# Kernel tuning notes

Measured on AMD Instinct MI355X. Metric: run time of the kernel, lower is better.

The kernel has to match this reference:

```python
import jax, jax.numpy as jnp
import numpy as np

B, T, F, H = 4, 2048, 512, 8
DK = F // H


def setup_inputs() -> dict:
    key = jax.random.key(0)
    ks = jax.random.split(key, 12)
    s = 1.0 / np.sqrt(F)
    return {
        "query": jax.random.normal(ks[0], (B, T, F), jnp.float32),
        "key": jax.random.normal(ks[1], (B, T, F), jnp.float32),
        "value": jax.random.normal(ks[2], (B, T, F), jnp.float32),
        "attn_mask": jax.random.randint(ks[3], (B, 1, T), 0, 2, jnp.int32),
        "Wq": jax.random.uniform(ks[4], (F, F), jnp.float32, -s, s),
        "bq": jax.random.uniform(ks[5], (F,), jnp.float32, -s, s),
        "Wk": jax.random.uniform(ks[6], (F, F), jnp.float32, -s, s),
        "bk": jax.random.uniform(ks[7], (F,), jnp.float32, -s, s),
        "Wv": jax.random.uniform(ks[8], (F, F), jnp.float32, -s, s),
        "bv": jax.random.uniform(ks[9], (F,), jnp.float32, -s, s),
        "Wo": jax.random.uniform(ks[10], (F, F), jnp.float32, -s, s),
        "bo": jax.random.uniform(ks[11], (F,), jnp.float32, -s, s),
    }


def reference(query, key, value, attn_mask, Wq, bq, Wk, bk, Wv, bv, Wo, bo):
    b = query.shape[0]
    # QKV projections -> (b, h, t, d_k)
    q = (query @ Wq.T + bq).reshape(b, -1, H, DK).transpose(0, 2, 1, 3)
    k = (key @ Wk.T + bk).reshape(b, -1, H, DK).transpose(0, 2, 1, 3)
    v = (value @ Wv.T + bv).reshape(b, -1, H, DK).transpose(0, 2, 1, 3)
    scores = jnp.einsum("bhqd,bhkd->bhqk", q, k) / np.sqrt(DK)
    # mask (b,1,t2) -> (b,1,1,t2); masked where mask == 0
    m = (attn_mask[:, None, :, :] == 0)
    min_val = jnp.finfo(scores.dtype).min
    scores = jnp.where(m, min_val, scores)
    attn = jnp.where(m, 0.0, jax.nn.softmax(scores, axis=-1))
    # dropout is identity in eval mode
    x = jnp.einsum("bhqk,bhkd->bhqd", attn, v)
    x = x.transpose(0, 2, 1, 3).reshape(b, -1, H * DK)
    return x @ Wo.T + bo
```

## Files before the change

kernel.cpp:

```cpp
#include <hip/hip_runtime.h>
#include <hip/hip_bf16.h>
#include <stdint.h>

#define B_ 4
#define T_ 2048
#define F_ 512
#define H_ 8
#define DK_ 64
#define BT_ (B_*T_)

typedef short bf16x8 __attribute__((ext_vector_type(8)));
typedef short s16x4 __attribute__((ext_vector_type(4)));
typedef float f32x4 __attribute__((ext_vector_type(4)));
typedef float f32x16 __attribute__((ext_vector_type(16)));

__device__ __forceinline__ unsigned short f2bf(float f) {
  union { float f; unsigned u; } v; v.f = f;
  return (unsigned short)((v.u + 0x7fffu + ((v.u >> 16) & 1u)) >> 16);
}

__device__ __forceinline__ unsigned cvtpk(float lo, float hi) {
  unsigned w;
  asm("v_cvt_pk_bf16_f32 %0, %1, %2" : "=v"(w) : "v"(lo), "v"(hi));
  return w;
}

__device__ __forceinline__ void gload_lds16(const void* g, void* l) {
  __builtin_amdgcn_global_load_lds((const __attribute__((address_space(1))) void*)g,
                                   (__attribute__((address_space(3))) void*)l, 16, 0, 0);
}

__global__ void convert_scan(const float* __restrict__ wq, const float* __restrict__ wk,
                             const float* __restrict__ wv, const float* __restrict__ wo,
                             const int* __restrict__ mask,
                             unsigned short* __restrict__ dst, int* __restrict__ invidx,
                             int* __restrict__ nbuf, float* __restrict__ maskf) {
  const int seg = blockIdx.y;
  const int tid = threadIdx.x;
  if (seg == 4) {
    if (blockIdx.x >= 4) return;
    const int b = blockIdx.x;
    __shared__ int cnt[256];
    const int base = b * T_ + tid * 8;
    int4 a = *(const int4*)(mask + base);
    int4 d = *(const int4*)(mask + base + 4);
    int m[8] = {a.x, a.y, a.z, a.w, d.x, d.y, d.z, d.w};
    int c = 0;
#pragma unroll
    for (int i = 0; i < 8; ++i) c += (m[i] != 0);
    cnt[tid] = c;
    __syncthreads();
    for (int off = 1; off < 256; off <<= 1) {
      int v = (tid >= off) ? cnt[tid - off] : 0;
      __syncthreads();
      cnt[tid] += v;
      __syncthreads();
    }
    int excl = cnt[tid] - c;
#pragma unroll
    for (int i = 0; i < 8; ++i)
      if (m[i]) { invidx[b * T_ + excl] = tid * 8 + i; ++excl; }
    const int nb = cnt[255];
    if (tid == 255) nbuf[b] = nb;
#pragma unroll
    for (int i = 0; i < 8; ++i) {
      const int j = tid * 8 + i;
      maskf[b * T_ + j] = (j < nb) ? 0.0f : -__builtin_inff();
    }
    return;
  }
  const float* src = seg == 0 ? wq : (seg == 1 ? wk : (seg == 2 ? wv : wo));
  unsigned short* out = dst + (size_t)seg * F_ * F_;
  const int idx = (blockIdx.x * 256 + tid) * 8;
  float4 a = *(const float4*)(src + idx);
  float4 b = *(const float4*)(src + idx + 4);
  union { unsigned w[4]; bf16x8 v; } t;
  t.w[0] = cvtpk(a.x, a.y); t.w[1] = cvtpk(a.z, a.w);
  t.w[2] = cvtpk(b.x, b.y); t.w[3] = cvtpk(b.z, b.w);
  *(bf16x8*)(out + idx) = t.v;
}

__global__ __launch_bounds__(256, 3) void gemm_qkv(
    const float* __restrict__ qin, const float* __restrict__ kin, const float* __restrict__ vin,
    const unsigned short* __restrict__ Wbase,
    const float* __restrict__ bq, const float* __restrict__ bk, const float* __restrict__ bv,
    const int* __restrict__ invidx, const int* __restrict__ nbuf,
    unsigned short* __restrict__ projq, unsigned short* __restrict__ kc,
    unsigned short* __restrict__ vt, float qscale) {
  const int id = blockIdx.x;
  const int p = id >> 8, l = id & 255;
  const int tid = threadIdx.x;
  const int wid = tid >> 6, lane = tid & 63;
  const int lr = lane & 15, lg = lane >> 4;
  const int wr = wid >> 1, wc = wid & 1;
  const int n0 = (l & 3) * 128;

  const float* Af;
  const float* bias;
  float sc = 1.0f;
  int obase, j0 = 0, b = 0, nb = T_;
  if (p == 0) {
    obase = (l >> 2) * 128;
    Af = qin; bias = bq; sc = qscale;
  } else {
    b = l >> 6;
    j0 = ((l >> 2) & 15) * 128;
    nb = nbuf[b];
    if (j0 >= ((nb + 63) & ~63)) return;
    obase = b * T_ + j0;
    Af = (p == 1) ? kin : vin;
    bias = (p == 1) ? bk : bv;
  }
  const unsigned short* W = Wbase + (size_t)p * F_ * F_;

  __shared__ __align__(16) unsigned short As[128 * 64];
  __shared__ __align__(16) unsigned short Bs[128 * 64];

  int srcrow[4];
#pragma unroll
  for (int i = 0; i < 4; ++i) {
    const int r = (i * 256 + tid) >> 3;
    if (p == 0) srcrow[i] = obase + r;
    else {
      int j = j0 + r;
      if (j >= nb) j = nb - 1;
      srcrow[i] = b * T_ + invidx[b * T_ + j];
    }
  }

  float4 aR[4][2];
  auto loadA = [&](int k0) {
#pragma unroll
    for (int i = 0; i < 4; ++i) {
      const int s = (i * 256 + tid) & 7;
      const float* sp = Af + (size_t)srcrow[i] * F_ + k0 + s * 8;
      aR[i][0] = *(const float4*)sp;
      aR[i][1] = *(const float4*)(sp + 4);
    }
  };
  auto writeA = [&]() {
#pragma unroll
    for (int i = 0; i < 4; ++i) {
      const int ch = i * 256 + tid;
      const int r = ch >> 3, s = ch & 7;
      union { unsigned w[4]; bf16x8 v; } t;
      t.w[0] = cvtpk(aR[i][0].x, aR[i][0].y); t.w[1] = cvtpk(aR[i][0].z, aR[i][0].w);
      t.w[2] = cvtpk(aR[i][1].x, aR[i][1].y); t.w[3] = cvtpk(aR[i][1].z, aR[i][1].w);
      *(bf16x8*)&As[r * 64 + ((s ^ (r & 7)) * 8)] = t.v;
    }
  };
  auto stageB = [&](int k0) {
#pragma unroll
    for (int i = 0; i < 4; ++i) {
      const int ch = i * 256 + tid;
      const int r = ch >> 3, s = ch & 7;
      gload_lds16(W + (size_t)(n0 + r) * F_ + k0 + ((s ^ (r & 7)) * 8),
                  &Bs[(i * 256 + wid * 64) * 8]);
    }
  };

  f32x4 acc[4][4] = {};
  loadA(0);
  for (int k0 = 0; k0 < F_; k0 += 64) {
    stageB(k0);
    writeA();
    __syncthreads();
    if (k0 + 64 < F_) loadA(k0 + 64);

#pragma unroll
    for (int kk = 0; kk < 2; ++kk) {
      bf16x8 af[4], bf[4];
      const int slotA = (kk * 4 + lg) ^ (lr & 7);
#pragma unroll
      for (int m = 0; m < 4; ++m)
        af[m] = *(const bf16x8*)&As[(wr * 64 + m * 16 + lr) * 64 + slotA * 8];
#pragma unroll
      for (int n = 0; n < 4; ++n)
        bf[n] = *(const bf16x8*)&Bs[(wc * 64 + n * 16 + lr) * 64 + slotA * 8];
#pragma unroll
      for (int m = 0; m < 4; ++m)
#pragma unroll
        for (int n = 0; n < 4; ++n)
          acc[m][n] = __builtin_amdgcn_mfma_f32_16x16x32_bf16(af[m], bf[n], acc[m][n], 0, 0, 0);
    }
    __syncthreads();
  }

  if (p == 2) {
#pragma unroll
    for (int n = 0; n < 4; ++n) {
      const int col = n0 + wc * 64 + n * 16 + lr;
      const float bvv = bias[col];
      unsigned short* vrow = vt + ((size_t)(b * 8 + (col >> 6)) * 64 + (col & 63)) * T_;
#pragma unroll
      for (int m = 0; m < 4; ++m) {
        const int kv = j0 + wr * 64 + m * 16 + lg * 4;
        union { unsigned short u[4]; s16x4 v; } ov;
#pragma unroll
        for (int j = 0; j < 4; ++j) ov.u[j] = f2bf(acc[m][n][j] + bvv);
        *(s16x4*)(vrow + kv) = ov.v;
      }
    }
  } else {
    unsigned short* outp = (p == 0) ? projq : kc;
#pragma unroll
    for (int n = 0; n < 4; ++n) {
      const int col = n0 + wc * 64 + n * 16 + lr;
      const float bvv = bias[col];
#pragma unroll
      for (int m = 0; m < 4; ++m) {
        const int rbase = obase + wr * 64 + m * 16 + lg * 4;
#pragma unroll
        for (int j = 0; j < 4; ++j)
          outp[(size_t)(rbase + j) * F_ + col] = f2bf((acc[m][n][j] + bvv) * sc);
      }
    }
  }
}

__global__ __launch_bounds__(256, 3) void gemm_out(
    const unsigned short* __restrict__ Abf, const unsigned short* __restrict__ W,
    const float* __restrict__ bias, float* __restrict__ outf) {
  const int l = blockIdx.x;
  const int m0 = (l >> 2) * 128, n0 = (l & 3) * 128;
  const int tid = threadIdx.x;
  const int wid = tid >> 6, lane = tid & 63;
  const int lr = lane & 15, lg = lane >> 4;
  const int wr = wid >> 1, wc = wid & 1;

  __shared__ __align__(16) unsigned short As[128 * 64];
  __shared__ __align__(16) unsigned short Bs[128 * 64];

  auto stage = [&](int k0) {
#pragma unroll
    for (int i = 0; i < 4; ++i) {
      const int ch = i * 256 + tid;
      const int r = ch >> 3, s = ch & 7;
      const int ks = ((s ^ (r & 7)) * 8);
      gload_lds16(Abf + (size_t)(m0 + r) * F_ + k0 + ks, &As[(i * 256 + wid * 64) * 8]);
      gload_lds16(W + (size_t)(n0 + r) * F_ + k0 + ks, &Bs[(i * 256 + wid * 64) * 8]);
    }
  };

  f32x4 acc[4][4] = {};
  for (int k0 = 0; k0 < F_; k0 += 64) {
    stage(k0);
    __syncthreads();
#pragma unroll
    for (int kk = 0; kk < 2; ++kk) {
      bf16x8 af[4], bf[4];
      const int slotA = (kk * 4 + lg) ^ (lr & 7);
#pragma unroll
      for (int m = 0; m < 4; ++m)
        af[m] = *(const bf16x8*)&As[(wr * 64 + m * 16 + lr) * 64 + slotA * 8];
#pragma unroll
      for (int n = 0; n < 4; ++n)
        bf[n] = *(const bf16x8*)&Bs[(wc * 64 + n * 16 + lr) * 64 + slotA * 8];
#pragma unroll
      for (int m = 0; m < 4; ++m)
#pragma unroll
        for (int n = 0; n < 4; ++n)
          acc[m][n] = __builtin_amdgcn_mfma_f32_16x16x32_bf16(af[m], bf[n], acc[m][n], 0, 0, 0);
    }
    __syncthreads();
  }

#pragma unroll
  for (int n = 0; n < 4; ++n) {
    const int col = n0 + wc * 64 + n * 16 + lr;
    const float bvv = bias[col];
#pragma unroll
    for (int m = 0; m < 4; ++m) {
      const int rbase = m0 + wr * 64 + m * 16 + lg * 4;
#pragma unroll
      for (int j = 0; j < 4; ++j)
        outf[(size_t)(rbase + j) * F_ + col] = acc[m][n][j] + bvv;
    }
  }
}

__global__ __launch_bounds__(256, 2) void attn_kernel(
    const unsigned short* __restrict__ Qp,
    const unsigned short* __restrict__ Kp,
    const unsigned short* __restrict__ Vt,
    const float* __restrict__ maskf,
    const int* __restrict__ nbuf,
    unsigned short* __restrict__ X) {
  const int tid = threadIdx.x, wid = tid >> 6, lane = tid & 63;
  const int la = lane & 31, hi = lane >> 5;
  const int id = blockIdx.x;
  const int swz = (id & 7) * 64 + (id >> 3);
  const int bh = swz >> 4, qb = swz & 15;
  const int b = bh >> 3, h = bh & 7;
  const int qrow = qb * 128 + wid * 32 + la;
  const int nt = (nbuf[b] + 127) >> 7;

  __shared__ __align__(16) unsigned short Ks[2][128 * 64];
  __shared__ __align__(16) unsigned short Vs[2][64 * 128];
  __shared__ __align__(16) float Ms[2][128];

  bf16x8 qf[4];
#pragma unroll
  for (int kk = 0; kk < 4; ++kk)
    qf[kk] = *(const bf16x8*)(Qp + (size_t)(b * T_ + qrow) * F_ + h * DK_ + kk * 16 + hi * 8);

  f32x16 oacc[2] = {};
  float mrun = -1e30f, lrun = 0.0f;

  auto stage = [&](int buf, int kv0) {
#pragma unroll
    for (int i = 0; i < 4; ++i) {
      const int ch = i * 256 + tid;
      const int r = ch >> 3, s = ch & 7;
      gload_lds16(Kp + (size_t)(b * T_ + kv0 + r) * F_ + h * DK_ + ((s ^ (r & 7)) * 8),
                  &Ks[buf][(i * 256 + wid * 64) * 8]);
      const int d = ch >> 4, s2 = ch & 15;
      gload_lds16(Vt + ((size_t)bh * DK_ + d) * T_ + kv0 + ((s2 ^ (d & 15)) * 8),
                  &Vs[buf][(i * 256 + wid * 64) * 8]);
    }
    if (wid == 0 && lane < 32)
      gload_lds16(maskf + b * T_ + kv0 + lane * 4, &Ms[buf][0]);
  };

  if (nt > 0) {
    stage(0, 0);
    __syncthreads();

    for (int t = 0; t < nt; ++t) {
      const int cur = t & 1;
      if (t < nt - 1) stage(cur ^ 1, (t + 1) * 128);

      f32x16 sb[4];
      __builtin_amdgcn_s_setprio(1);
#pragma unroll
      for (int n = 0; n < 4; ++n) {
        bf16x8 kf[4];
#pragma unroll
        for (int kk = 0; kk < 4; ++kk)
          kf[kk] = *(const bf16x8*)&Ks[cur][(n * 32 + la) * 64 + ((((kk << 1) | hi) ^ (la & 7)) * 8)];
        f32x16 s = {};
#pragma unroll
        for (int kk = 0; kk < 4; ++kk)
          s = __builtin_amdgcn_mfma_f32_32x32x16_bf16(kf[kk], qf[kk], s, 0, 0, 0);
        sb[n] = s;
      }
      __builtin_amdgcn_s_setprio(0);

      f32x4 mfv[4][4];
#pragma unroll
      for (int n = 0; n < 4; ++n)
#pragma unroll
        for (int g = 0; g < 4; ++g)
          mfv[n][g] = *(const f32x4*)&Ms[cur][n * 32 + 8 * g + 4 * hi];

      float mx[16];
#pragma unroll
      for (int r = 0; r < 16; ++r)
        mx[r] = fmaxf(fmaxf(sb[0][r], sb[1][r]), fmaxf(sb[2][r], sb[3][r]));
#pragma unroll
      for (int st = 8; st > 0; st >>= 1)
#pragma unroll
        for (int r = 0; r < st; ++r) mx[r] = fmaxf(mx[r], mx[r + st]);
      const float rmx = fmaxf(mx[0], __shfl_xor(mx[0], 32, 64));

      if (!__all(rmx <= mrun + 8.0f)) {
        const float mnew = fmaxf(mrun, rmx);
        const float alpha = __builtin_amdgcn_exp2f(mrun - mnew);
        lrun *= alpha;
#pragma unroll
        for (int m = 0; m < 2; ++m)
#pragma unroll
          for (int r = 0; r < 16; ++r) oacc[m][r] *= alpha;
        mrun = mnew;
      }

#pragma unroll
      for (int n = 0; n < 4; ++n)
#pragma unroll
        for (int r = 0; r < 16; ++r)
          sb[n][r] = __builtin_amdgcn_exp2f((sb[n][r] + mfv[n][r >> 2][r & 3]) - mrun);

      float sm[16];
#pragma unroll
      for (int r = 0; r < 16; ++r)
        sm[r] = (sb[0][r] + sb[1][r]) + (sb[2][r] + sb[3][r]);
#pragma unroll
      for (int st = 8; st > 0; st >>= 1)
#pragma unroll
        for (int r = 0; r < st; ++r) sm[r] += sm[r + st];
      lrun += sm[0] + __shfl_xor(sm[0], 32, 64);

      unsigned lowr[4][2][2], uppr[4][2][2];
#pragma unroll
      for (int n = 0; n < 4; ++n)
#pragma unroll
        for (int gg = 0; gg < 2; ++gg)
#pragma unroll
          for (int hh = 0; hh < 2; ++hh) {
            unsigned xE = cvtpk(sb[n][4 * (2 * gg) + 2 * hh], sb[n][4 * (2 * gg) + 2 * hh + 1]);
            unsigned xO = cvtpk(sb[n][4 * (2 * gg + 1) + 2 * hh], sb[n][4 * (2 * gg + 1) + 2 * hh + 1]);
            asm("v_permlane32_swap_b32 %0, %1" : "+v"(xE), "+v"(xO));
            lowr[n][gg][hh] = xE;
            uppr[n][gg][hh] = xO;
          }

#pragma unroll
      for (int kt = 0; kt < 8; ++kt) {
        const int n = kt >> 1, gg = kt & 1;
        union { unsigned w[4]; bf16x8 v; } pf;
        pf.w[0] = lowr[n][gg][0]; pf.w[1] = lowr[n][gg][1];
        pf.w[2] = uppr[n][gg][0]; pf.w[3] = uppr[n][gg][1];
        __builtin_amdgcn_s_setprio(1);
#pragma unroll
        for (int m = 0; m < 2; ++m) {
          const int d = m * 32 + la;
          bf16x8 vfr = *(const bf16x8*)&Vs[cur][d * 128 + ((((kt << 1) | hi) ^ (d & 15)) * 8)];
          oacc[m] = __builtin_amdgcn_mfma_f32_32x32x16_bf16(vfr, pf.v, oacc[m], 0, 0, 0);
        }
        __builtin_amdgcn_s_setprio(0);
      }
      __syncthreads();
    }
  }

  const float inv = 1.0f / fmaxf(lrun, 1e-37f);
#pragma unroll
  for (int m = 0; m < 2; ++m)
#pragma unroll
    for (int g = 0; g < 4; ++g) {
      union { unsigned short u[4]; s16x4 v; } ov;
#pragma unroll
      for (int j = 0; j < 4; ++j) ov.u[j] = f2bf(oacc[m][4 * g + j] * inv);
      *(s16x4*)(X + (size_t)(b * T_ + qrow) * F_ + h * DK_ + m * 32 + 8 * g + 4 * hi) = ov.v;
    }
}

extern "C" void kernel_launch(void* const* d_in, const int* in_sizes, int n_in,
                              void* d_out, int out_size, void* d_ws, size_t ws_size,
                              hipStream_t stream) {
  const float* q  = (const float*)d_in[0];
  const float* k  = (const float*)d_in[1];
  const float* v  = (const float*)d_in[2];
  const int* mask = (const int*)d_in[3];
  const float* Wq = (const float*)d_in[4];
  const float* bq = (const float*)d_in[5];
  const float* Wk = (const float*)d_in[6];
  const float* bk = (const float*)d_in[7];
  const float* Wv = (const float*)d_in[8];
  const float* bv = (const float*)d_in[9];
  const float* Wo = (const float*)d_in[10];
  const float* bo = (const float*)d_in[11];
  float* out = (float*)d_out;

  unsigned short* ws = (unsigned short*)d_ws;
  unsigned short* wts   = ws;
  unsigned short* projq = wts + (size_t)4 * F_ * F_;
  unsigned short* kc    = projq + (size_t)BT_ * F_;
  unsigned short* vt    = kc + (size_t)BT_ * F_;
  unsigned short* xbuf  = vt + (size_t)BT_ * F_;
  float* maskf = (float*)(xbuf + (size_t)BT_ * F_);
  int* invidx  = (int*)(maskf + BT_);
  int* nbuf    = invidx + BT_;

  const float kQScale = 0.18033688011112042f;

  convert_scan<<<dim3(128, 5, 1), 256, 0, stream>>>(
      Wq, Wk, Wv, Wo, mask, wts, invidx, nbuf, maskf);
  gemm_qkv<<<dim3(768, 1, 1), 256, 0, stream>>>(
      q, k, v, wts, bq, bk, bv, invidx, nbuf, projq, kc, vt, kQScale);
  attn_kernel<<<dim3(512, 1, 1), 256, 0, stream>>>(
      projq, kc, vt, maskf, nbuf, xbuf);
  gemm_out<<<dim3(256, 1, 1), 256, 0, stream>>>(
      xbuf, wts + (size_t)3 * F_ * F_, bo, out);
}
```

Baseline: 83.60 us.

## Load K/V fragments directly from global in attention; drop mask buffer, swizzle GEMM blocks

The attention kernel no longer stages K and V tiles through double-buffered LDS. Each wave now loads its MFMA fragments straight from global memory into registers and does no block-level barriers. The precomputed float mask buffer is removed and replaced by an in-register tail check against the compacted key count. Both GEMM kernels also get an XCD-aware block-index swizzle to improve L2 locality. The trade-off is that every wave re-reads K/V from global/L2 instead of sharing them through LDS, and register pressure goes up.

```diff
diff --git a/kernel.cpp b/kernel.cpp
--- a/kernel.cpp
+++ b/kernel.cpp
@@ -34,7 +34,7 @@
                              const float* __restrict__ wv, const float* __restrict__ wo,
                              const int* __restrict__ mask,
                              unsigned short* __restrict__ dst, int* __restrict__ invidx,
-                             int* __restrict__ nbuf, float* __restrict__ maskf) {
+                             int* __restrict__ nbuf) {
   const int seg = blockIdx.y;
   const int tid = threadIdx.x;
   if (seg == 4) {
@@ -60,13 +60,7 @@
 #pragma unroll
     for (int i = 0; i < 8; ++i)
       if (m[i]) { invidx[b * T_ + excl] = tid * 8 + i; ++excl; }
-    const int nb = cnt[255];
-    if (tid == 255) nbuf[b] = nb;
-#pragma unroll
-    for (int i = 0; i < 8; ++i) {
-      const int j = tid * 8 + i;
-      maskf[b * T_ + j] = (j < nb) ? 0.0f : -__builtin_inff();
-    }
+    if (tid == 255) nbuf[b] = cnt[255];
     return;
   }
   const float* src = seg == 0 ? wq : (seg == 1 ? wk : (seg == 2 ? wv : wo));
@@ -87,7 +81,8 @@
     const int* __restrict__ invidx, const int* __restrict__ nbuf,
     unsigned short* __restrict__ projq, unsigned short* __restrict__ kc,
     unsigned short* __restrict__ vt, float qscale) {
-  const int id = blockIdx.x;
+  const int id0 = blockIdx.x;
+  const int id = (id0 & 7) * 96 + (id0 >> 3);
   const int p = id >> 8, l = id & 255;
   const int tid = threadIdx.x;
   const int wid = tid >> 6, lane = tid & 63;
@@ -221,7 +216,8 @@
 __global__ __launch_bounds__(256, 3) void gemm_out(
     const unsigned short* __restrict__ Abf, const unsigned short* __restrict__ W,
     const float* __restrict__ bias, float* __restrict__ outf) {
-  const int l = blockIdx.x;
+  const int id0 = blockIdx.x;
+  const int l = (id0 & 7) * 32 + (id0 >> 3);
   const int m0 = (l >> 2) * 128, n0 = (l & 3) * 128;
   const int tid = threadIdx.x;
   const int wid = tid >> 6, lane = tid & 63;
@@ -283,7 +279,6 @@
     const unsigned short* __restrict__ Qp,
     const unsigned short* __restrict__ Kp,
     const unsigned short* __restrict__ Vt,
-    const float* __restrict__ maskf,
     const int* __restrict__ nbuf,
     unsigned short* __restrict__ X) {
   const int tid = threadIdx.x, wid = tid >> 6, lane = tid & 63;
@@ -293,11 +288,11 @@
   const int bh = swz >> 4, qb = swz & 15;
   const int b = bh >> 3, h = bh & 7;
   const int qrow = qb * 128 + wid * 32 + la;
-  const int nt = (nbuf[b] + 127) >> 7;
-
-  __shared__ __align__(16) unsigned short Ks[2][128 * 64];
-  __shared__ __align__(16) unsigned short Vs[2][64 * 128];
-  __shared__ __align__(16) float Ms[2][128];
+  const int nb = nbuf[b];
+  const int nt = (nb + 127) >> 7;
+
+  const unsigned short* Kbase = Kp + (size_t)b * T_ * F_ + h * DK_;
+  const unsigned short* Vbase = Vt + (size_t)bh * DK_ * T_;
 
   bf16x8 qf[4];
 #pragma unroll
@@ -307,119 +302,108 @@
   f32x16 oacc[2] = {};
   float mrun = -1e30f, lrun = 0.0f;
 
-  auto stage = [&](int buf, int kv0) {
-#pragma unroll
-    for (int i = 0; i < 4; ++i) {
-      const int ch = i * 256 + tid;
-      const int r = ch >> 3, s = ch & 7;
-      gload_lds16(Kp + (size_t)(b * T_ + kv0 + r) * F_ + h * DK_ + ((s ^ (r & 7)) * 8),
-                  &Ks[buf][(i * 256 + wid * 64) * 8]);
-      const int d = ch >> 4, s2 = ch & 15;
-      gload_lds16(Vt + ((size_t)bh * DK_ + d) * T_ + kv0 + ((s2 ^ (d & 15)) * 8),
-                  &Vs[buf][(i * 256 + wid * 64) * 8]);
-    }
-    if (wid == 0 && lane < 32)
-      gload_lds16(maskf + b * T_ + kv0 + lane * 4, &Ms[buf][0]);
-  };
-
-  if (nt > 0) {
-    stage(0, 0);
-    __syncthreads();
-
-    for (int t = 0; t < nt; ++t) {
-      const int cur = t & 1;
-      if (t < nt - 1) stage(cur ^ 1, (t + 1) * 128);
-
-      f32x16 sb[4];
+  for (int t = 0; t < nt; ++t) {
+    const int kv0 = t * 128;
+
+    bf16x8 kf[4][4];
+#pragma unroll
+    for (int n = 0; n < 4; ++n)
+#pragma unroll
+      for (int kk = 0; kk < 4; ++kk)
+        kf[n][kk] = *(const bf16x8*)(Kbase + (size_t)(kv0 + n * 32 + la) * F_ + kk * 16 + hi * 8);
+
+    f32x16 sb[4];
+    __builtin_amdgcn_s_setprio(1);
+#pragma unroll
+    for (int n = 0; n < 4; ++n) {
+      f32x16 s = {};
+#pragma unroll
+      for (int kk = 0; kk < 4; ++kk)
+        s = __builtin_amdgcn_mfma_f32_32x32x16_bf16(kf[n][kk], qf[kk], s, 0, 0, 0);
+      sb[n] = s;
+    }
+    __builtin_amdgcn_s_setprio(0);
+
+    bf16x8 vf[2][8];
+#pragma unroll
+    for (int m = 0; m < 2; ++m)
+#pragma unroll
+      for (int kt = 0; kt < 8; ++kt)
+        vf[m][kt] = *(const bf16x8*)(Vbase + (size_t)(m * 32 + la) * T_ + kv0 + kt * 16 + hi * 8);
+
+    if (kv0 + 128 > nb) {
+      const int kvb = kv0 + 4 * hi;
+#pragma unroll
+      for (int n = 0; n < 4; ++n)
+#pragma unroll
+        for (int r = 0; r < 16; ++r) {
+          const int kv = kvb + n * 32 + (r & 3) + 8 * (r >> 2);
+          if (kv >= nb) sb[n][r] = -__builtin_inff();
+        }
+    }
+
+    float mx[16];
+#pragma unroll
+    for (int r = 0; r < 16; ++r)
+      mx[r] = fmaxf(fmaxf(sb[0][r], sb[1][r]), fmaxf(sb[2][r], sb[3][r]));
+#pragma unroll
+    for (int st = 8; st > 0; st >>= 1)
+#pragma unroll
+      for (int r = 0; r < st; ++r) mx[r] = fmaxf(mx[r], mx[r + st]);
+    const float rmx = fmaxf(mx[0], __shfl_xor(mx[0], 32, 64));
+
+    if (!__all(rmx <= mrun + 8.0f)) {
+      const float mnew = fmaxf(mrun, rmx);
+      const float alpha = __builtin_amdgcn_exp2f(mrun - mnew);
+      lrun *= alpha;
+#pragma unroll
+      for (int m = 0; m < 2; ++m)
+#pragma unroll
+        for (int r = 0; r < 16; ++r) oacc[m][r] *= alpha;
+      mrun = mnew;
+    }
+
+#pragma unroll
+    for (int n = 0; n < 4; ++n)
+#pragma unroll
+      for (int r = 0; r < 16; ++r)
+        sb[n][r] = __builtin_amdgcn_exp2f(sb[n][r] - mrun);
+
+    float sm[16];
+#pragma unroll
+    for (int r = 0; r < 16; ++r)
+      sm[r] = (sb[0][r] + sb[1][r]) + (sb[2][r] + sb[3][r]);
+#pragma unroll
+    for (int st = 8; st > 0; st >>= 1)
+#pragma unroll
+      for (int r = 0; r < st; ++r) sm[r] += sm[r + st];
+    lrun += sm[0] + __shfl_xor(sm[0], 32, 64);
+
+    unsigned lowr[4][2][2], uppr[4][2][2];
+#pragma unroll
+    for (int n = 0; n < 4; ++n)
+#pragma unroll
+      for (int gg = 0; gg < 2; ++gg)
+#pragma unroll
+        for (int hh = 0; hh < 2; ++hh) {
+          unsigned xE = cvtpk(sb[n][4 * (2 * gg) + 2 * hh], sb[n][4 * (2 * gg) + 2 * hh + 1]);
+          unsigned xO = cvtpk(sb[n][4 * (2 * gg + 1) + 2 * hh], sb[n][4 * (2 * gg + 1) + 2 * hh + 1]);
+          asm("v_permlane32_swap_b32 %0, %1" : "+v"(xE), "+v"(xO));
+          lowr[n][gg][hh] = xE;
+          uppr[n][gg][hh] = xO;
+        }
+
+#pragma unroll
+    for (int kt = 0; kt < 8; ++kt) {
+      const int n = kt >> 1, gg = kt & 1;
+      union { unsigned w[4]; bf16x8 v; } pf;
+      pf.w[0] = lowr[n][gg][0]; pf.w[1] = lowr[n][gg][1];
+      pf.w[2] = uppr[n][gg][0]; pf.w[3] = uppr[n][gg][1];
       __builtin_amdgcn_s_setprio(1);
 #pragma unroll
-      for (int n = 0; n < 4; ++n) {
-        bf16x8 kf[4];
-#pragma unroll
-        for (int kk = 0; kk < 4; ++kk)
-          kf[kk] = *(const bf16x8*)&Ks[cur][(n * 32 + la) * 64 + ((((kk << 1) | hi) ^ (la & 7)) * 8)];
-        f32x16 s = {};
-#pragma unroll
-        for (int kk = 0; kk < 4; ++kk)
-          s = __builtin_amdgcn_mfma_f32_32x32x16_bf16(kf[kk], qf[kk], s, 0, 0, 0);
-        sb[n] = s;
-      }
+      for (int m = 0; m < 2; ++m)
+        oacc[m] = __builtin_amdgcn_mfma_f32_32x32x16_bf16(vf[m][kt], pf.v, oacc[m], 0, 0, 0);
       __builtin_amdgcn_s_setprio(0);
-
-      f32x4 mfv[4][4];
-#pragma unroll
-      for (int n = 0; n < 4; ++n)
-#pragma unroll
-        for (int g = 0; g < 4; ++g)
-          mfv[n][g] = *(const f32x4*)&Ms[cur][n * 32 + 8 * g + 4 * hi];
-
-      float mx[16];
-#pragma unroll
-      for (int r = 0; r < 16; ++r)
-        mx[r] = fmaxf(fmaxf(sb[0][r], sb[1][r]), fmaxf(sb[2][r], sb[3][r]));
-#pragma unroll
-      for (int st = 8; st > 0; st >>= 1)
-#pragma unroll
-        for (int r = 0; r < st; ++r) mx[r] = fmaxf(mx[r], mx[r + st]);
-      const float rmx = fmaxf(mx[0], __shfl_xor(mx[0], 32, 64));
-
-      if (!__all(rmx <= mrun + 8.0f)) {
-        const float mnew = fmaxf(mrun, rmx);
-        const float alpha = __builtin_amdgcn_exp2f(mrun - mnew);
-        lrun *= alpha;
-#pragma unroll
-        for (int m = 0; m < 2; ++m)
-#pragma unroll
-          for (int r = 0; r < 16; ++r) oacc[m][r] *= alpha;
-        mrun = mnew;
-      }
-
-#pragma unroll
-      for (int n = 0; n < 4; ++n)
-#pragma unroll
-        for (int r = 0; r < 16; ++r)
-          sb[n][r] = __builtin_amdgcn_exp2f((sb[n][r] + mfv[n][r >> 2][r & 3]) - mrun);
-
-      float sm[16];
-#pragma unroll
-      for (int r = 0; r < 16; ++r)
-        sm[r] = (sb[0][r] + sb[1][r]) + (sb[2][r] + sb[3][r]);
-#pragma unroll
-      for (int st = 8; st > 0; st >>= 1)
-#pragma unroll
-        for (int r = 0; r < st; ++r) sm[r] += sm[r + st];
-      lrun += sm[0] + __shfl_xor(sm[0], 32, 64);
-
-      unsigned lowr[4][2][2], uppr[4][2][2];
-#pragma unroll
-      for (int n = 0; n < 4; ++n)
-#pragma unroll
-        for (int gg = 0; gg < 2; ++gg)
-#pragma unroll
-          for (int hh = 0; hh < 2; ++hh) {
-            unsigned xE = cvtpk(sb[n][4 * (2 * gg) + 2 * hh], sb[n][4 * (2 * gg) + 2 * hh + 1]);
-            unsigned xO = cvtpk(sb[n][4 * (2 * gg + 1) + 2 * hh], sb[n][4 * (2 * gg + 1) + 2 * hh + 1]);
-            asm("v_permlane32_swap_b32 %0, %1" : "+v"(xE), "+v"(xO));
-            lowr[n][gg][hh] = xE;
-            uppr[n][gg][hh] = xO;
-          }
-
-#pragma unroll
-      for (int kt = 0; kt < 8; ++kt) {
-        const int n = kt >> 1, gg = kt & 1;
-        union { unsigned w[4]; bf16x8 v; } pf;
-        pf.w[0] = lowr[n][gg][0]; pf.w[1] = lowr[n][gg][1];
-        pf.w[2] = uppr[n][gg][0]; pf.w[3] = uppr[n][gg][1];
-        __builtin_amdgcn_s_setprio(1);
-#pragma unroll
-        for (int m = 0; m < 2; ++m) {
-          const int d = m * 32 + la;
-          bf16x8 vfr = *(const bf16x8*)&Vs[cur][d * 128 + ((((kt << 1) | hi) ^ (d & 15)) * 8)];
-          oacc[m] = __builtin_amdgcn_mfma_f32_32x32x16_bf16(vfr, pf.v, oacc[m], 0, 0, 0);
-        }
-        __builtin_amdgcn_s_setprio(0);
-      }
-      __syncthreads();
     }
   }
 
@@ -458,18 +442,17 @@
   unsigned short* kc    = projq + (size_t)BT_ * F_;
   unsigned short* vt    = kc + (size_t)BT_ * F_;
   unsigned short* xbuf  = vt + (size_t)BT_ * F_;
-  float* maskf = (float*)(xbuf + (size_t)BT_ * F_);
-  int* invidx  = (int*)(maskf + BT_);
+  int* invidx  = (int*)(xbuf + (size_t)BT_ * F_);
   int* nbuf    = invidx + BT_;
 
   const float kQScale = 0.18033688011112042f;
 
   convert_scan<<<dim3(128, 5, 1), 256, 0, stream>>>(
-      Wq, Wk, Wv, Wo, mask, wts, invidx, nbuf, maskf);
+      Wq, Wk, Wv, Wo, mask, wts, invidx, nbuf);
   gemm_qkv<<<dim3(768, 1, 1), 256, 0, stream>>>(
       q, k, v, wts, bq, bk, bv, invidx, nbuf, projq, kc, vt, kQScale);
   attn_kernel<<<dim3(512, 1, 1), 256, 0, stream>>>(
-      projq, kc, vt, maskf, nbuf, xbuf);
+      projq, kc, vt, nbuf, xbuf);
   gemm_out<<<dim3(256, 1, 1), 256, 0, stream>>>(
       xbuf, wts + (size_t)3 * F_ * F_, bo, out);
 }
```

Result: slower. 112.9 us (+35.0%).
